# Performance work log

Hardware: AMD Instinct MI355X
Metric: run time of the kernel (lower is better)

## Reference

```python
import jax, jax.numpy as jnp
import numpy as np

LN_EPS = 1e-5

def layernorm(x, w, b):
    # LayerNorm over last dim (head_dim), affine
    mu = jnp.mean(x, axis=-1, keepdims=True)
    var = jnp.mean(jnp.square(x - mu), axis=-1, keepdims=True)
    return (x - mu) * jax.lax.rsqrt(var + LN_EPS) * w + b

def setup_inputs() -> dict:
    key = jax.random.key(0)
    ks = jax.random.split(key, 6)
    B, N, C, H = 2, 2048, 1024, 16
    hd = C // H
    s = 1.0 / np.sqrt(C)
    return {
        "x": jax.random.normal(ks[0], (B, N, C), jnp.float32),
        "W_qkv": jax.random.normal(ks[1], (C, 3 * C), jnp.float32) * s,  # qkv_bias=False
        "qn_w": jnp.ones((hd,), jnp.float32),
        "qn_b": jnp.zeros((hd,), jnp.float32),
        "kn_w": jnp.ones((hd,), jnp.float32),
        "kn_b": jnp.zeros((hd,), jnp.float32),
        "W_proj": jax.random.normal(ks[2], (C, C), jnp.float32) * s,
        "b_proj": jnp.zeros((C,), jnp.float32),
    }

def reference(x, W_qkv, qn_w, qn_b, kn_w, kn_b, W_proj, b_proj):
    B, N, C = x.shape
    H = 16
    hd = C // H
    scale = hd ** -0.5
    qkv = (x @ W_qkv).reshape(B, N, 3, H, hd)
    qkv = jnp.transpose(qkv, (2, 0, 3, 1, 4))  # [3,B,H,N,hd]
    q, k, v = qkv[0], qkv[1], qkv[2]
    q = layernorm(q, qn_w, qn_b)
    k = layernorm(k, kn_w, kn_b)
    q = q * scale
    attn = jnp.einsum('bhnd,bhmd->bhnm', q, k)  # [B,H,N,N]
    attn = jax.nn.softmax(attn, axis=-1)  # attn_drop p=0 -> identity
    o = jnp.einsum('bhnm,bhmd->bhnd', attn, v)
    o = jnp.transpose(o, (0, 2, 1, 3)).reshape(B, N, C)
    return o @ W_proj + b_proj  # proj_drop p=0 -> identity
```

## Files before the change

kernel.cpp:

```cpp
#include <hip/hip_runtime.h>
#include <hip/hip_bf16.h>

#define B_  2
#define N_  2048
#define C_  1024
#define H_  16
#define HD_ 64
#define QSZ (B_*N_*C_)
#define QSCALE 0.18033688011112042f

typedef __attribute__((ext_vector_type(8))) short short8;
typedef __attribute__((ext_vector_type(4))) float floatx4;

__device__ __forceinline__ unsigned short f2bf(float f) {
    unsigned int u = __builtin_bit_cast(unsigned int, f);
    u += 0x7fff + ((u >> 16) & 1);
    return (unsigned short)(u >> 16);
}
__device__ __forceinline__ unsigned int pk2bf(float a, float b) {
    unsigned int ua = __builtin_bit_cast(unsigned int, a);
    unsigned int ub = __builtin_bit_cast(unsigned int, b);
    ua += 0x7fff + ((ua >> 16) & 1);
    ub += 0x7fff + ((ub >> 16) & 1);
    return __builtin_amdgcn_perm(ub, ua, 0x07060302);
}

__device__ __forceinline__ void g2l16(const void* g, void* l) {
    __builtin_amdgcn_global_load_lds(
        (const __attribute__((address_space(1))) void*)g,
        (__attribute__((address_space(3))) void*)l, 16, 0, 0);
}

__global__ __launch_bounds__(256) void pack_bf16_kernel(
    const float* __restrict__ src, unsigned short* __restrict__ dst)
{
    const int i = blockIdx.x * 256 + threadIdx.x;
    float4 v = ((const float4*)src)[i];
    ushort4 o = {f2bf(v.x), f2bf(v.y), f2bf(v.z), f2bf(v.w)};
    ((ushort4*)dst)[i] = o;
}

__global__ __launch_bounds__(256) void transpose_pack2_kernel(
    const float* __restrict__ Wq, unsigned short* __restrict__ Wqt,
    const float* __restrict__ Wp, unsigned short* __restrict__ Wpt)
{
    __shared__ unsigned short tl[32][34];
    const bool isq = blockIdx.x < 96;
    const int bx = isq ? blockIdx.x : blockIdx.x - 96;
    const int Nd = isq ? 3072 : 1024;
    const float* W = isq ? Wq : Wp;
    unsigned short* Wt = isq ? Wqt : Wpt;
    const int r  = threadIdx.x >> 3;
    const int c4 = (threadIdx.x & 7) * 4;
    const int n0 = bx * 32, k0 = blockIdx.y * 32;
    float4 v = *(const float4*)&W[(size_t)(k0 + r) * Nd + n0 + c4];
    tl[r][c4 + 0] = f2bf(v.x); tl[r][c4 + 1] = f2bf(v.y);
    tl[r][c4 + 2] = f2bf(v.z); tl[r][c4 + 3] = f2bf(v.w);
    __syncthreads();
    ushort4 o = {tl[c4 + 0][r], tl[c4 + 1][r], tl[c4 + 2][r], tl[c4 + 3][r]};
    *(ushort4*)&Wt[(size_t)(n0 + r) * 1024 + k0 + c4] = o;
}

#define GEMM_CORE(A_, Bt_, Kd_, row0_, col0_)                                 \
    __shared__ unsigned short As[128 * 32];                                   \
    __shared__ unsigned short Bs[128 * 32];                                   \
    const int t    = threadIdx.x;                                             \
    const int lane = t & 63;                                                  \
    const int w    = t >> 6;                                                  \
    const int l15  = lane & 15;                                               \
    const int quad = lane >> 4;                                               \
    const int wm   = w >> 1, wn = w & 1;                                      \
    size_t aOff = (size_t)(row0_ + w * 16 + (lane >> 2)) * Kd_ + (lane & 3) * 8; \
    size_t bOff = (size_t)(col0_ + w * 16 + (lane >> 2)) * Kd_ + (lane & 3) * 8; \
    floatx4 acc[4][4];                                                        \
    _Pragma("unroll")                                                         \
    for (int i = 0; i < 4; ++i)                                               \
        _Pragma("unroll")                                                     \
        for (int j = 0; j < 4; ++j) acc[i][j] = floatx4{0.f, 0.f, 0.f, 0.f};  \
    for (int k0 = 0; k0 < Kd_; k0 += 32) {                                    \
        _Pragma("unroll")                                                     \
        for (int c = 0; c < 2; ++c) {                                         \
            g2l16(&A_[aOff + (size_t)c * 64 * Kd_ + k0],                      \
                  &As[(w * 16 + c * 64) * 32]);                               \
            g2l16(&Bt_[bOff + (size_t)c * 64 * Kd_ + k0],                     \
                  &Bs[(w * 16 + c * 64) * 32]);                               \
        }                                                                     \
        __syncthreads();                                                      \
        short8 af[4], bf[4];                                                  \
        _Pragma("unroll")                                                     \
        for (int i = 0; i < 4; ++i)                                           \
            af[i] = *(const short8*)&As[(wm * 64 + i * 16 + l15) * 32 + quad * 8]; \
        _Pragma("unroll")                                                     \
        for (int j = 0; j < 4; ++j)                                           \
            bf[j] = *(const short8*)&Bs[(wn * 64 + j * 16 + l15) * 32 + quad * 8]; \
        _Pragma("unroll")                                                     \
        for (int i = 0; i < 4; ++i)                                           \
            _Pragma("unroll")                                                 \
            for (int j = 0; j < 4; ++j)                                       \
                acc[i][j] = __builtin_amdgcn_mfma_f32_16x16x32_bf16(          \
                    af[i], bf[j], acc[i][j], 0, 0, 0);                        \
        __syncthreads();                                                      \
    }

__global__ __launch_bounds__(256) void gemm_qkv_kernel(
    const unsigned short* __restrict__ X,
    const unsigned short* __restrict__ Wt,
    const float* __restrict__ qn_w, const float* __restrict__ qn_b,
    const float* __restrict__ kn_w, const float* __restrict__ kn_b,
    unsigned short* __restrict__ qb, unsigned short* __restrict__ kb,
    unsigned short* __restrict__ vb)
{
    const int row0 = blockIdx.y * 128;
    const int col0 = blockIdx.x * 128;
    GEMM_CORE(X, Wt, 1024, row0, col0)
    const int which = col0 >> 10;
    const int h = ((col0 & 1023) >> 6) + wn;
    if (which == 2) {
        #pragma unroll
        for (int j = 0; j < 4; ++j) {
            const int d = j * 16 + l15;
            #pragma unroll
            for (int i = 0; i < 4; ++i) {
                #pragma unroll
                for (int r = 0; r < 4; ++r) {
                    const int grow = row0 + wm * 64 + i * 16 + quad * 4 + r;
                    const int bidx = grow >> 11, n = grow & 2047;
                    vb[(((size_t)(bidx * H_ + h) * N_ + n) * HD_) + d] =
                        f2bf(acc[i][j][r]);
                }
            }
        }
    } else {
        const float* wt = (which == 0) ? qn_w : kn_w;
        const float* bi = (which == 0) ? qn_b : kn_b;
        unsigned short* dstbuf = (which == 0) ? qb : kb;
        float w4[4], b4[4];
        #pragma unroll
        for (int j = 0; j < 4; ++j) {
            w4[j] = wt[j * 16 + l15];
            b4[j] = bi[j * 16 + l15];
        }
        #pragma unroll
        for (int i = 0; i < 4; ++i) {
            #pragma unroll
            for (int r = 0; r < 4; ++r) {
                float v0 = acc[i][0][r], v1 = acc[i][1][r],
                      v2 = acc[i][2][r], v3 = acc[i][3][r];
                float s = (v0 + v1) + (v2 + v3);
                #pragma unroll
                for (int o = 1; o < 16; o <<= 1) s += __shfl_xor(s, o);
                const float mu = s * (1.0f / 64.0f);
                const float d0 = v0 - mu, d1 = v1 - mu,
                            d2 = v2 - mu, d3 = v3 - mu;
                float s2 = (d0 * d0 + d1 * d1) + (d2 * d2 + d3 * d3);
                #pragma unroll
                for (int o = 1; o < 16; o <<= 1) s2 += __shfl_xor(s2, o);
                const float rstd = rsqrtf(s2 * (1.0f / 64.0f) + 1e-5f);
                float y0 = d0 * rstd * w4[0] + b4[0];
                float y1 = d1 * rstd * w4[1] + b4[1];
                float y2 = d2 * rstd * w4[2] + b4[2];
                float y3 = d3 * rstd * w4[3] + b4[3];
                if (which == 0) {
                    y0 *= QSCALE; y1 *= QSCALE; y2 *= QSCALE; y3 *= QSCALE;
                }
                const int grow = row0 + wm * 64 + i * 16 + quad * 4 + r;
                const int bidx = grow >> 11, n = grow & 2047;
                unsigned short* dp =
                    &dstbuf[(((size_t)(bidx * H_ + h) * N_ + n) * HD_) + l15];
                dp[0]  = f2bf(y0);
                dp[16] = f2bf(y1);
                dp[32] = f2bf(y2);
                dp[48] = f2bf(y3);
            }
        }
    }
}

__global__ __launch_bounds__(256) void gemm_proj_kernel(
    const unsigned short* __restrict__ O,
    const unsigned short* __restrict__ Wt,
    const float* __restrict__ bias, float* __restrict__ out)
{
    __shared__ unsigned short As[64 * 32];
    __shared__ unsigned short Bs[128 * 32];
    const int t    = threadIdx.x;
    const int lane = t & 63;
    const int w    = t >> 6;
    const int l15  = lane & 15;
    const int quad = lane >> 4;
    const int row0 = blockIdx.y * 64;
    const int col0 = blockIdx.x * 128;
    size_t aOff = (size_t)(row0 + w * 16 + (lane >> 2)) * 1024 + (lane & 3) * 8;
    size_t bOff = (size_t)(col0 + w * 16 + (lane >> 2)) * 1024 + (lane & 3) * 8;
    floatx4 acc[4][2];
    #pragma unroll
    for (int i = 0; i < 4; ++i)
        #pragma unroll
        for (int j = 0; j < 2; ++j) acc[i][j] = floatx4{0.f, 0.f, 0.f, 0.f};
    for (int k0 = 0; k0 < 1024; k0 += 32) {
        g2l16(&O[aOff + k0], &As[(w * 16) * 32]);
        #pragma unroll
        for (int c = 0; c < 2; ++c)
            g2l16(&Wt[bOff + (size_t)c * 64 * 1024 + k0],
                  &Bs[(w * 16 + c * 64) * 32]);
        __syncthreads();
        short8 af[4], bf[2];
        #pragma unroll
        for (int i = 0; i < 4; ++i)
            af[i] = *(const short8*)&As[(i * 16 + l15) * 32 + quad * 8];
        #pragma unroll
        for (int j = 0; j < 2; ++j)
            bf[j] = *(const short8*)&Bs[(w * 32 + j * 16 + l15) * 32 + quad * 8];
        #pragma unroll
        for (int i = 0; i < 4; ++i)
            #pragma unroll
            for (int j = 0; j < 2; ++j)
                acc[i][j] = __builtin_amdgcn_mfma_f32_16x16x32_bf16(
                    af[i], bf[j], acc[i][j], 0, 0, 0);
        __syncthreads();
    }
    #pragma unroll
    for (int j = 0; j < 2; ++j) {
        const int gcol = col0 + w * 32 + j * 16 + l15;
        const float b = bias[gcol];
        #pragma unroll
        for (int i = 0; i < 4; ++i) {
            #pragma unroll
            for (int r = 0; r < 4; ++r) {
                const int grow = row0 + i * 16 + quad * 4 + r;
                out[(size_t)grow * 1024 + gcol] = acc[i][j][r] + b;
            }
        }
    }
}

__global__ __launch_bounds__(256, 2) void flash_kernel(
    const unsigned short* __restrict__ qb, const unsigned short* __restrict__ kb,
    const unsigned short* __restrict__ vb, unsigned short* __restrict__ ob)
{
    __shared__ __align__(16) unsigned short Ks[128 * 72];
    __shared__ __align__(16) unsigned short Vt[64 * 136];
    __shared__ __align__(16) unsigned short Pb[128 * 136];
    __shared__ float Lb[128];
    const int t    = threadIdx.x;
    const int lane = t & 63;
    const int w    = t >> 6;
    const int qg   = w & 1;
    const int kvh  = w >> 1;
    const int l15  = lane & 15;
    const int quad = lane >> 4;
    const int q0   = blockIdx.x * 128;
    const int bh   = blockIdx.y;
    const unsigned short* Q = qb + (size_t)bh * N_ * HD_;
    const unsigned short* K = kb + (size_t)bh * N_ * HD_;
    const unsigned short* V = vb + (size_t)bh * N_ * HD_;

    {
        const int r = t >> 3, c = (t & 7) * 8;
        #pragma unroll
        for (int rep = 0; rep < 4; ++rep)
            *(short8*)&Pb[(rep * 32 + r) * 136 + c] =
                *(const short8*)&Q[(size_t)(q0 + rep * 32 + r) * 64 + c];
    }
    __syncthreads();
    short8 qf[4][2];
    #pragma unroll
    for (int qt = 0; qt < 4; ++qt)
        #pragma unroll
        for (int kk = 0; kk < 2; ++kk)
            qf[qt][kk] = *(const short8*)
                &Pb[(qg * 64 + qt * 16 + l15) * 136 + kk * 32 + quad * 8];

    floatx4 acc[4][4];
    #pragma unroll
    for (int qt = 0; qt < 4; ++qt)
        #pragma unroll
        for (int dt = 0; dt < 4; ++dt) acc[qt][dt] = floatx4{0.f, 0.f, 0.f, 0.f};
    float l_part[4] = {0.f, 0.f, 0.f, 0.f};

    const int kr = t & 127, kc = (t >> 7) * 32;
    const int vkv = (t & 63) * 2, vd = (t >> 6) * 16;

    short8 kR[4], vR[4];
    #pragma unroll
    for (int c = 0; c < 4; ++c)
        kR[c] = *(const short8*)&K[(size_t)kr * 64 + kc + c * 8];
    vR[0] = *(const short8*)&V[(size_t)vkv * 64 + vd];
    vR[1] = *(const short8*)&V[(size_t)vkv * 64 + vd + 8];
    vR[2] = *(const short8*)&V[(size_t)(vkv + 1) * 64 + vd];
    vR[3] = *(const short8*)&V[(size_t)(vkv + 1) * 64 + vd + 8];

    for (int kt = 0; kt < N_; kt += 128) {
        __syncthreads();
        #pragma unroll
        for (int c = 0; c < 4; ++c)
            *(short8*)&Ks[kr * 72 + kc + c * 8] = kR[c];
        #pragma unroll
        for (int j = 0; j < 8; ++j) {
            unsigned int p0 = (unsigned int)(unsigned short)vR[0][j] |
                              ((unsigned int)(unsigned short)vR[2][j] << 16);
            unsigned int p1 = (unsigned int)(unsigned short)vR[1][j] |
                              ((unsigned int)(unsigned short)vR[3][j] << 16);
            *(unsigned int*)&Vt[(vd + j) * 136 + vkv]     = p0;
            *(unsigned int*)&Vt[(vd + 8 + j) * 136 + vkv] = p1;
        }
        __syncthreads();
        if (kt + 128 < N_) {
            const int kt2 = kt + 128;
            #pragma unroll
            for (int c = 0; c < 4; ++c)
                kR[c] = *(const short8*)&K[(size_t)(kt2 + kr) * 64 + kc + c * 8];
            vR[0] = *(const short8*)&V[(size_t)(kt2 + vkv) * 64 + vd];
            vR[1] = *(const short8*)&V[(size_t)(kt2 + vkv) * 64 + vd + 8];
            vR[2] = *(const short8*)&V[(size_t)(kt2 + vkv + 1) * 64 + vd];
            vR[3] = *(const short8*)&V[(size_t)(kt2 + vkv + 1) * 64 + vd + 8];
        }

        #pragma unroll
        for (int ci = 0; ci < 4; ++ci) {
            const int ct = kvh * 4 + ci;
            short8 a0 = *(const short8*)&Ks[(ct * 16 + l15) * 72 + quad * 8];
            short8 a1 = *(const short8*)&Ks[(ct * 16 + l15) * 72 + 32 + quad * 8];
            #pragma unroll
            for (int qt = 0; qt < 4; ++qt) {
                floatx4 s = {0.f, 0.f, 0.f, 0.f};
                s = __builtin_amdgcn_mfma_f32_16x16x32_bf16(a0, qf[qt][0], s, 0, 0, 0);
                s = __builtin_amdgcn_mfma_f32_16x16x32_bf16(a1, qf[qt][1], s, 0, 0, 0);
                const float p0 = __builtin_amdgcn_exp2f(s[0]);
                const float p1 = __builtin_amdgcn_exp2f(s[1]);
                const float p2 = __builtin_amdgcn_exp2f(s[2]);
                const float p3 = __builtin_amdgcn_exp2f(s[3]);
                l_part[qt] += (p0 + p1) + (p2 + p3);
                uint2 pk;
                pk.x = pk2bf(p0, p1);
                pk.y = pk2bf(p2, p3);
                *(uint2*)&Pb[(qg * 64 + qt * 16 + l15) * 136 + ct * 16 + quad * 4] = pk;
            }
        }
        asm volatile("" ::: "memory");

        #pragma unroll
        for (int kk2 = 0; kk2 < 2; ++kk2) {
            const int kk = kvh * 2 + kk2;
            short8 pbf[4];
            #pragma unroll
            for (int qt = 0; qt < 4; ++qt)
                pbf[qt] = *(const short8*)
                    &Pb[(qg * 64 + qt * 16 + l15) * 136 + kk * 32 + quad * 8];
            #pragma unroll
            for (int dt = 0; dt < 4; ++dt) {
                short8 va = *(const short8*)
                    &Vt[(dt * 16 + l15) * 136 + kk * 32 + quad * 8];
                #pragma unroll
                for (int qt = 0; qt < 4; ++qt)
                    acc[qt][dt] = __builtin_amdgcn_mfma_f32_16x16x32_bf16(
                        va, pbf[qt], acc[qt][dt], 0, 0, 0);
            }
        }
    }

    #pragma unroll
    for (int qt = 0; qt < 4; ++qt) {
        l_part[qt] += __shfl_xor(l_part[qt], 16);
        l_part[qt] += __shfl_xor(l_part[qt], 32);
    }
    __syncthreads();
    float* Pf = (float*)Pb;
    if (kvh == 0) {
        #pragma unroll
        for (int qt = 0; qt < 4; ++qt) {
            const int q = qg * 64 + qt * 16 + l15;
            #pragma unroll
            for (int dt = 0; dt < 4; ++dt)
                #pragma unroll
                for (int r = 0; r < 4; ++r)
                    Pf[q * 68 + dt * 16 + quad * 4 + r] = acc[qt][dt][r];
            if (quad == 0) Lb[q] = l_part[qt];
        }
    }
    __syncthreads();
    if (kvh == 1) {
        #pragma unroll
        for (int qt = 0; qt < 4; ++qt) {
            const int q = qg * 64 + qt * 16 + l15;
            #pragma unroll
            for (int dt = 0; dt < 4; ++dt)
                #pragma unroll
                for (int r = 0; r < 4; ++r)
                    Pf[q * 68 + dt * 16 + quad * 4 + r] += acc[qt][dt][r];
            if (quad == 0) Lb[q] += l_part[qt];
        }
    }
    __syncthreads();
    {
        const int orow = t >> 1, oc = (t & 1) * 32;
        const float inv = 1.0f / Lb[orow];
        const int bidx = bh >> 4, h = bh & 15;
        unsigned short* dst =
            &ob[((size_t)(bidx * N_ + q0 + orow)) * C_ + h * 64 + oc];
        #pragma unroll
        for (int k = 0; k < 4; ++k) {
            float4 f0 = *(float4*)&Pf[orow * 68 + oc + k * 8];
            float4 f1 = *(float4*)&Pf[orow * 68 + oc + k * 8 + 4];
            uint4 u;
            u.x = pk2bf(f0.x * inv, f0.y * inv);
            u.y = pk2bf(f0.z * inv, f0.w * inv);
            u.z = pk2bf(f1.x * inv, f1.y * inv);
            u.w = pk2bf(f1.z * inv, f1.w * inv);
            *(uint4*)&dst[k * 8] = u;
        }
    }
}

extern "C" void kernel_launch(void* const* d_in, const int* in_sizes, int n_in,
                              void* d_out, int out_size, void* d_ws, size_t ws_size,
                              hipStream_t stream) {
    const float* x      = (const float*)d_in[0];
    const float* W_qkv  = (const float*)d_in[1];
    const float* qn_w   = (const float*)d_in[2];
    const float* qn_b   = (const float*)d_in[3];
    const float* kn_w   = (const float*)d_in[4];
    const float* kn_b   = (const float*)d_in[5];
    const float* W_proj = (const float*)d_in[6];
    const float* b_proj = (const float*)d_in[7];
    float* out = (float*)d_out;

    unsigned short* qb  = (unsigned short*)d_ws;
    unsigned short* kb  = qb + (size_t)QSZ;
    unsigned short* vb  = kb + (size_t)QSZ;
    unsigned short* ob  = vb + (size_t)QSZ;
    unsigned short* xb  = ob + (size_t)B_ * N_ * C_;
    unsigned short* wqt = xb + (size_t)B_ * N_ * C_;
    unsigned short* wpt = wqt + (size_t)3 * C_ * C_;

    pack_bf16_kernel<<<dim3((B_ * N_ * C_) / 1024), 256, 0, stream>>>(x, xb);
    transpose_pack2_kernel<<<dim3(128, 32), 256, 0, stream>>>(W_qkv, wqt, W_proj, wpt);
    gemm_qkv_kernel<<<dim3(24, 32), 256, 0, stream>>>(
        xb, wqt, qn_w, qn_b, kn_w, kn_b, qb, kb, vb);
    flash_kernel<<<dim3(N_ / 128, B_ * H_), 256, 0, stream>>>(qb, kb, vb, ob);
    gemm_proj_kernel<<<dim3(8, 64), 256, 0, stream>>>(ob, wpt, b_proj, out);
}
```

Measured before the change: 202.1 us.

## Split flash attention KV tile across four wave pairs with 512-thread blocks

The flash kernel moves from 256 to 512 threads per block. Each 128-key tile is now split into four 32-key quarters, one per wave pair, instead of two halves, so each wave does half the MFMA work per tile. K/V staging and the Q load are redistributed so every thread loads less. The final cross-wave reduction of the partial outputs becomes a three-phase serialized accumulate with extra barriers. This adds more waves per CU to hide latency, at the cost of more synchronization and reduction overhead and higher register pressure under launch_bounds(512,4).

Result: slower. 417.0 us (+106.3%).

```diff
diff --git a/kernel.cpp b/kernel.cpp
--- a/kernel.cpp
+++ b/kernel.cpp
@@ -234,7 +234,7 @@
     }
 }
 
-__global__ __launch_bounds__(256, 2) void flash_kernel(
+__global__ __launch_bounds__(512, 4) void flash_kernel(
     const unsigned short* __restrict__ qb, const unsigned short* __restrict__ kb,
     const unsigned short* __restrict__ vb, unsigned short* __restrict__ ob)
 {
@@ -246,7 +246,7 @@
     const int lane = t & 63;
     const int w    = t >> 6;
     const int qg   = w & 1;
-    const int kvh  = w >> 1;
+    const int kvq  = w >> 1;
     const int l15  = lane & 15;
     const int quad = lane >> 4;
     const int q0   = blockIdx.x * 128;
@@ -257,10 +257,10 @@
 
     {
         const int r = t >> 3, c = (t & 7) * 8;
-        #pragma unroll
-        for (int rep = 0; rep < 4; ++rep)
-            *(short8*)&Pb[(rep * 32 + r) * 136 + c] =
-                *(const short8*)&Q[(size_t)(q0 + rep * 32 + r) * 64 + c];
+        *(short8*)&Pb[r * 136 + c] =
+            *(const short8*)&Q[(size_t)(q0 + r) * 64 + c];
+        *(short8*)&Pb[(r + 64) * 136 + c] =
+            *(const short8*)&Q[(size_t)(q0 + r + 64) * 64 + c];
     }
     __syncthreads();
     short8 qf[4][2];
@@ -278,47 +278,37 @@
         for (int dt = 0; dt < 4; ++dt) acc[qt][dt] = floatx4{0.f, 0.f, 0.f, 0.f};
     float l_part[4] = {0.f, 0.f, 0.f, 0.f};
 
-    const int kr = t & 127, kc = (t >> 7) * 32;
-    const int vkv = (t & 63) * 2, vd = (t >> 6) * 16;
-
-    short8 kR[4], vR[4];
-    #pragma unroll
-    for (int c = 0; c < 4; ++c)
-        kR[c] = *(const short8*)&K[(size_t)kr * 64 + kc + c * 8];
+    const int kr = t >> 2, kc = (t & 3) * 16;
+    const int vkv = (t & 63) * 2, vd = (t >> 6) * 8;
+
+    short8 kR[2], vR[2];
+    kR[0] = *(const short8*)&K[(size_t)kr * 64 + kc];
+    kR[1] = *(const short8*)&K[(size_t)kr * 64 + kc + 8];
     vR[0] = *(const short8*)&V[(size_t)vkv * 64 + vd];
-    vR[1] = *(const short8*)&V[(size_t)vkv * 64 + vd + 8];
-    vR[2] = *(const short8*)&V[(size_t)(vkv + 1) * 64 + vd];
-    vR[3] = *(const short8*)&V[(size_t)(vkv + 1) * 64 + vd + 8];
+    vR[1] = *(const short8*)&V[(size_t)(vkv + 1) * 64 + vd];
 
     for (int kt = 0; kt < N_; kt += 128) {
         __syncthreads();
-        #pragma unroll
-        for (int c = 0; c < 4; ++c)
-            *(short8*)&Ks[kr * 72 + kc + c * 8] = kR[c];
+        *(short8*)&Ks[kr * 72 + kc]     = kR[0];
+        *(short8*)&Ks[kr * 72 + kc + 8] = kR[1];
         #pragma unroll
         for (int j = 0; j < 8; ++j) {
-            unsigned int p0 = (unsigned int)(unsigned short)vR[0][j] |
-                              ((unsigned int)(unsigned short)vR[2][j] << 16);
-            unsigned int p1 = (unsigned int)(unsigned short)vR[1][j] |
-                              ((unsigned int)(unsigned short)vR[3][j] << 16);
-            *(unsigned int*)&Vt[(vd + j) * 136 + vkv]     = p0;
-            *(unsigned int*)&Vt[(vd + 8 + j) * 136 + vkv] = p1;
+            unsigned int pk = (unsigned int)(unsigned short)vR[0][j] |
+                              ((unsigned int)(unsigned short)vR[1][j] << 16);
+            *(unsigned int*)&Vt[(vd + j) * 136 + vkv] = pk;
         }
         __syncthreads();
         if (kt + 128 < N_) {
             const int kt2 = kt + 128;
-            #pragma unroll
-            for (int c = 0; c < 4; ++c)
-                kR[c] = *(const short8*)&K[(size_t)(kt2 + kr) * 64 + kc + c * 8];
+            kR[0] = *(const short8*)&K[(size_t)(kt2 + kr) * 64 + kc];
+            kR[1] = *(const short8*)&K[(size_t)(kt2 + kr) * 64 + kc + 8];
             vR[0] = *(const short8*)&V[(size_t)(kt2 + vkv) * 64 + vd];
-            vR[1] = *(const short8*)&V[(size_t)(kt2 + vkv) * 64 + vd + 8];
-            vR[2] = *(const short8*)&V[(size_t)(kt2 + vkv + 1) * 64 + vd];
-            vR[3] = *(const short8*)&V[(size_t)(kt2 + vkv + 1) * 64 + vd + 8];
-        }
-
-        #pragma unroll
-        for (int ci = 0; ci < 4; ++ci) {
-            const int ct = kvh * 4 + ci;
+            vR[1] = *(const short8*)&V[(size_t)(kt2 + vkv + 1) * 64 + vd];
+        }
+
+        #pragma unroll
+        for (int ci = 0; ci < 2; ++ci) {
+            const int ct = kvq * 2 + ci;
             short8 a0 = *(const short8*)&Ks[(ct * 16 + l15) * 72 + quad * 8];
             short8 a1 = *(const short8*)&Ks[(ct * 16 + l15) * 72 + 32 + quad * 8];
             #pragma unroll
@@ -339,9 +329,8 @@
         }
         asm volatile("" ::: "memory");
 
-        #pragma unroll
-        for (int kk2 = 0; kk2 < 2; ++kk2) {
-            const int kk = kvh * 2 + kk2;
+        {
+            const int kk = kvq;
             short8 pbf[4];
             #pragma unroll
             for (int qt = 0; qt < 4; ++qt)
@@ -366,48 +355,48 @@
     }
     __syncthreads();
     float* Pf = (float*)Pb;
-    if (kvh == 0) {
+    if (kvq == 0) {
         #pragma unroll
         for (int qt = 0; qt < 4; ++qt) {
             const int q = qg * 64 + qt * 16 + l15;
             #pragma unroll
             for (int dt = 0; dt < 4; ++dt)
+                *(floatx4*)&Pf[q * 68 + dt * 16 + quad * 4] = acc[qt][dt];
+            if (quad == 0) Lb[q] = l_part[qt];
+        }
+    }
+    __syncthreads();
+    #pragma unroll
+    for (int ph = 1; ph < 4; ++ph) {
+        if (kvq == ph) {
+            #pragma unroll
+            for (int qt = 0; qt < 4; ++qt) {
+                const int q = qg * 64 + qt * 16 + l15;
                 #pragma unroll
-                for (int r = 0; r < 4; ++r)
-                    Pf[q * 68 + dt * 16 + quad * 4 + r] = acc[qt][dt][r];
-            if (quad == 0) Lb[q] = l_part[qt];
-        }
-    }
-    __syncthreads();
-    if (kvh == 1) {
-        #pragma unroll
-        for (int qt = 0; qt < 4; ++qt) {
-            const int q = qg * 64 + qt * 16 + l15;
-            #pragma unroll
-            for (int dt = 0; dt < 4; ++dt)
-                #pragma unroll
-                for (int r = 0; r < 4; ++r)
-                    Pf[q * 68 + dt * 16 + quad * 4 + r] += acc[qt][dt][r];
-            if (quad == 0) Lb[q] += l_part[qt];
-        }
-    }
-    __syncthreads();
+                for (int dt = 0; dt < 4; ++dt) {
+                    floatx4 cur = *(floatx4*)&Pf[q * 68 + dt * 16 + quad * 4];
+                    *(floatx4*)&Pf[q * 68 + dt * 16 + quad * 4] = cur + acc[qt][dt];
+                }
+                if (quad == 0) Lb[q] += l_part[qt];
+            }
+        }
+        __syncthreads();
+    }
     {
-        const int orow = t >> 1, oc = (t & 1) * 32;
-        const float inv = 1.0f / Lb[orow];
+        const int r = t >> 3, c = (t & 7) * 8;
         const int bidx = bh >> 4, h = bh & 15;
-        unsigned short* dst =
-            &ob[((size_t)(bidx * N_ + q0 + orow)) * C_ + h * 64 + oc];
-        #pragma unroll
-        for (int k = 0; k < 4; ++k) {
-            float4 f0 = *(float4*)&Pf[orow * 68 + oc + k * 8];
-            float4 f1 = *(float4*)&Pf[orow * 68 + oc + k * 8 + 4];
+        #pragma unroll
+        for (int rep = 0; rep < 2; ++rep) {
+            const int row = r + rep * 64;
+            const float inv = 1.0f / Lb[row];
+            float4 f0 = *(float4*)&Pf[row * 68 + c];
+            float4 f1 = *(float4*)&Pf[row * 68 + c + 4];
             uint4 u;
             u.x = pk2bf(f0.x * inv, f0.y * inv);
             u.y = pk2bf(f0.z * inv, f0.w * inv);
             u.z = pk2bf(f1.x * inv, f1.y * inv);
             u.w = pk2bf(f1.z * inv, f1.w * inv);
-            *(uint4*)&dst[k * 8] = u;
+            *(uint4*)&ob[((size_t)(bidx * N_ + q0 + row)) * C_ + h * 64 + c] = u;
         }
     }
 }
@@ -437,6 +426,6 @@
     transpose_pack2_kernel<<<dim3(128, 32), 256, 0, stream>>>(W_qkv, wqt, W_proj, wpt);
     gemm_qkv_kernel<<<dim3(24, 32), 256, 0, stream>>>(
         xb, wqt, qn_w, qn_b, kn_w, kn_b, qb, kb, vb);
-    flash_kernel<<<dim3(N_ / 128, B_ * H_), 256, 0, stream>>>(qb, kb, vb, ob);
+    flash_kernel<<<dim3(N_ / 128, B_ * H_), 512, 0, stream>>>(qb, kb, vb, ob);
     gemm_proj_kernel<<<dim3(8, 64), 256, 0, stream>>>(ob, wpt, b_proj, out);
 }
```
